# Optimization experiments

Measured on AMD Instinct MI355X. Metric: run time of the kernel, lower is better.

## Reference

```python
import jax, jax.numpy as jnp
import numpy as np

EPS = 1e-5


def _conv1x1_3d(x, w, b):
    # x: [B,C,T,H,W], w: [O,C], b: [O]  (Conv3d with kernel 1)
    return jnp.einsum('bcthw,oc->bothw', x, w) + b[None, :, None, None, None]


def _nonlocal_layer(x, Kw, Kb, Qw, Qb, Vw, Vb, Ow, Ob, gamma, beta, in_dim):
    K = _conv1x1_3d(x, Kw, Kb)
    Q = _conv1x1_3d(x, Qw, Qb)
    V = _conv1x1_3d(x, Vw, Vb)
    B, C, T, H, W = K.shape
    S = T * H * W
    Kf = K.reshape(B, C, S)
    Qf = Q.reshape(B, C, S)
    Vf = V.reshape(B, C, S)
    # KQ[b,s,t] = sum_c K[b,c,s] Q[b,c,t];  attn = softmax over t
    attn = jax.nn.softmax(jnp.einsum('bcs,bct->bst', Kf, Qf) / np.sqrt(in_dim).astype(np.float32), axis=2)
    # original broadcast pattern: (V.view(B,C,S,1) * attn[:,None]).sum(3)
    #   == V[b,c,s] * sum_t attn[b,s,t]  (rows of softmax sum to ~1)
    Vn = Vf * attn.sum(axis=2)[:, None, :]
    Vn = jax.nn.relu(Vn).reshape(B, C, T, H, W)
    O = jax.nn.relu(_conv1x1_3d(Vn, Ow, Ob))
    y = x + O
    # BatchNorm3d in training mode: per-channel batch statistics
    mu = y.mean(axis=(0, 2, 3, 4), keepdims=True)
    var = y.var(axis=(0, 2, 3, 4), keepdims=True)
    return gamma[None, :, None, None, None] * (y - mu) / jnp.sqrt(var + EPS) + beta[None, :, None, None, None]


def _conv_transpose_2x2_s2(x, w, b):
    # torch ConvTranspose2d(k=2, stride=2): weight [Cin, Cout, 2, 2]; output pixels don't overlap
    N, C, H, W = x.shape
    O = w.shape[1]
    y = jnp.einsum('nchw,codk->nohdwk', x, w).reshape(N, O, 2 * H, 2 * W)
    return y + b[None, :, None, None]


def _positional_encoding(S, D):
    position = jnp.arange(S, dtype=jnp.float32)[:, None]
    div_term = jnp.exp(jnp.arange(0, D, 2, dtype=jnp.float32) * (-np.log(10000.0) / D))
    pe = jnp.zeros((S, D), dtype=jnp.float32)
    pe = pe.at[:, 0::2].set(jnp.sin(position * div_term))
    pe = pe.at[:, 1::2].set(jnp.cos(position * div_term))
    return pe  # [S, D]


def setup_inputs() -> dict:
    key = jax.random.key(0)
    ks = jax.random.split(key, 24)
    B, Tc, Hc, Wc = 8, 6, 12, 12
    Tf, Hf, Wf = 4, 12, 12
    Din, Dff, Dout, L = 1024, 512, 128, 2
    s = 0.02
    inp = {
        'context': jax.random.normal(ks[0], (B, Tc, Din, Hc, Wc), jnp.float32),
        'frame': jax.random.normal(ks[1], (B, Tf, Din, Hf, Wf), jnp.float32),
        'nl_Kw': jax.random.normal(ks[2], (L, Dff, Din), jnp.float32) * s,
        'nl_Kb': jnp.zeros((L, Dff), jnp.float32),
        'nl_Qw': jax.random.normal(ks[3], (L, Dff, Din), jnp.float32) * s,
        'nl_Qb': jnp.zeros((L, Dff), jnp.float32),
        'nl_Vw': jax.random.normal(ks[4], (L, Dff, Din), jnp.float32) * s,
        'nl_Vb': jnp.zeros((L, Dff), jnp.float32),
        'nl_Ow': jax.random.normal(ks[5], (L, Din, Dff), jnp.float32) * s,
        'nl_Ob': jnp.zeros((L, Din), jnp.float32),
        'nl_gamma': jnp.ones((L, Din), jnp.float32),
        'nl_beta': jnp.zeros((L, Din), jnp.float32),
        'tp_w': jax.random.normal(ks[6], (Dout, Din, 3, 3, 3), jnp.float32) * s,
        'tp_b': jnp.zeros((Dout,), jnp.float32),
        'up1_w': jax.random.normal(ks[7], (Din, Dff, 2, 2), jnp.float32) * s,
        'up1_b': jnp.zeros((Dff,), jnp.float32),
        'up2_w': jax.random.normal(ks[8], (Dff, Dout, 2, 2), jnp.float32) * s,
        'up2_b': jnp.zeros((Dout,), jnp.float32),
    }
    return inp


def reference(context, frame, nl_Kw, nl_Kb, nl_Qw, nl_Qb, nl_Vw, nl_Vb, nl_Ow, nl_Ob,
              nl_gamma, nl_beta, tp_w, tp_b, up1_w, up1_b, up2_w, up2_b):
    in_dim = context.shape[2]
    out_dim = up2_w.shape[1]
    # ---- non-local layers over context ----
    x = jnp.swapaxes(context, 1, 2)  # [B, C, T, H, W]
    n_layers = nl_Kw.shape[0]
    for l in range(n_layers):
        x = _nonlocal_layer(x, nl_Kw[l], nl_Kb[l], nl_Qw[l], nl_Qb[l], nl_Vw[l], nl_Vb[l],
                            nl_Ow[l], nl_Ob[l], nl_gamma[l], nl_beta[l], in_dim)
    # ---- temporal pool (Conv3d k=3, VALID) + ReLU + global avg pool ----
    g = jax.lax.conv_general_dilated(x, tp_w, (1, 1, 1), 'VALID',
                                     dimension_numbers=('NCDHW', 'OIDHW', 'NCDHW'))
    g = jax.nn.relu(g + tp_b[None, :, None, None, None])
    goal_embed = g.mean(axis=(2, 3, 4))  # [B, out_dim]
    # ---- upsample frame ----
    B, Tf, C, H, W = frame.shape
    fr = frame.reshape(B * Tf, C, H, W)
    h = jax.nn.relu(_conv_transpose_2x2_s2(fr, up1_w, up1_b))
    h = _conv_transpose_2x2_s2(h, up2_w, up2_b)  # [B*Tf, out_dim, 4H, 4W]
    N = B * Tf
    S = H * W * 16
    state_embed = h.reshape(N, out_dim, S)
    # ---- positional encoding on V ----
    pe = _positional_encoding(S, out_dim)  # [S, D]
    V = jnp.transpose(state_embed, (0, 2, 1)) + pe[None, :, :]  # [N, S, D]
    # ---- goal/state attention (note: torch .repeat tiles t-major, kept faithful) ----
    goal_rep = jnp.tile(goal_embed, (Tf, 1))  # [Tf*B, D], index t*B+b
    SG = jnp.einsum('nds,nd->ns', state_embed, goal_rep) / np.sqrt(out_dim).astype(np.float32)
    attn = jax.nn.softmax(SG, axis=1)  # [N, S]
    state_goal_attn = jnp.einsum('ns,nsd->nd', attn, V).reshape(B, Tf, out_dim)
    return (goal_embed, state_goal_attn)
```

## Files before the change

kernel.cpp:

```cpp
#include <hip/hip_runtime.h>
#include <cstddef>
#include <cstdint>


static constexpr int B_ = 8, TC = 6, TF = 4, DIN = 1024, DFF = 512, DOUT = 128;
static constexpr int HWP = 144;
static constexpr int P_CTX = B_ * TC * HWP;
static constexpr int NF = B_ * TF;
static constexpr int P_FRM = NF * HWP;
static constexpr int P_H1 = NF * 24 * 24;
static constexpr int P_H2 = NF * 48 * 48;
static constexpr int S2 = 48 * 48;
static constexpr int NPOS = 3200;

static constexpr size_t OFF_XB   = 0;
static constexpr size_t OFF_YB   = 3538944;
static constexpr size_t OFF_VNB  = 7077888;
static constexpr size_t OFF_WB1  = 8847360;
static constexpr size_t OFF_WB2  = 9371648;
static constexpr size_t OFF_ST   = 9895936;
static constexpr size_t OFF_TWB  = 9900032;
static constexpr size_t OFF_W1B  = 11669504;
static constexpr size_t OFF_W2B  = 12718080;
static constexpr size_t OFF_GP   = 12849152;
static constexpr size_t OFF_R    = 18378752;
static constexpr size_t OFF_HP1B = 18788352;
static constexpr size_t OFF_F0B  = 23506944;
static constexpr size_t OFF_HP2B = 0;
static constexpr size_t OFF_SG   = 12849152;
static constexpr size_t OFF_PE   = 7077888;

typedef __attribute__((ext_vector_type(8))) short bf16x8;
typedef __attribute__((ext_vector_type(4))) float f32x4;
typedef __attribute__((ext_vector_type(4))) unsigned short us4;
typedef __attribute__((ext_vector_type(8))) unsigned short us8;

__device__ __forceinline__ unsigned short f2b(float f) {
    union { float f; uint32_t u; } x{f};
    uint32_t r = x.u + 0x7FFFu + ((x.u >> 16) & 1u);
    return (unsigned short)(r >> 16);
}
__device__ __forceinline__ float b2f(unsigned short u) {
    union { uint32_t u; float f; } x;
    x.u = (uint32_t)u << 16;
    return x.f;
}

#define GL16(g, s)                                                        \
    __builtin_amdgcn_global_load_lds(                                     \
        (const __attribute__((address_space(1))) void*)(g),               \
        (__attribute__((address_space(3))) void*)(s), 16, 0, 0)

static constexpr int PW0 = 4 * 524288;
static constexpr int PW1 = PW0 + 27 * 1024 * 128;
static constexpr int PW2 = PW1 + 4 * 512 * 1024;
static constexpr int PW3 = PW2 + 4 * 128 * 512;
static constexpr int NB_PREP = PW3 / 256;
static constexpr int NB_CTXT = 9 * 16 * (B_ * TC);
static constexpr int NB_FRMT = 9 * 16 * NF;

__device__ __forceinline__ void transpose_body(const float* __restrict__ in,
                                               unsigned short* __restrict__ outB,
                                               int C, int HW, int bx, int by, int bz,
                                               float (*T)[17]) {
    int tid = threadIdx.x;
    int tx = tid & 15, ty = tid >> 4;
    int f = bz, hw0 = bx * 16, c0 = by * 64;
#pragma unroll
    for (int i = 0; i < 4; ++i)
        T[ty + 16 * i][tx] = in[((size_t)f * C + c0 + ty + 16 * i) * HW + hw0 + tx];
    __syncthreads();
#pragma unroll
    for (int i = 0; i < 4; ++i)
        outB[((size_t)f * HW + hw0 + ty) * C + c0 + tx + 16 * i] = f2b(T[tx + 16 * i][ty]);
}

__global__ __launch_bounds__(256) void prep_all(
    const float* __restrict__ Vw, const float* __restrict__ Ow,
    const float* __restrict__ tp, const float* __restrict__ u1w,
    const float* __restrict__ u2w,
    const float* __restrict__ context, const float* __restrict__ frame,
    unsigned short* __restrict__ WB1, unsigned short* __restrict__ WB2,
    unsigned short* __restrict__ TWB, unsigned short* __restrict__ W1B,
    unsigned short* __restrict__ W2B,
    unsigned short* __restrict__ XB, unsigned short* __restrict__ F0B) {
    __shared__ float T[64][17];
    int b = blockIdx.x;
    if (b < NB_PREP) {
        int t = b * 256 + threadIdx.x;
        if (t < PW0) {
            int which = t >> 19;
            int r = t & 524287;
            int kr = r & 7;
            int layer = which >> 1;
            if ((which & 1) == 0) {
                int o = (r >> 3) & 511, kg = (r >> 3) >> 9;
                WB1[(size_t)layer * 524288 + r] =
                    f2b(Vw[(size_t)layer * 524288 + (size_t)o * 1024 + kg * 8 + kr]);
            } else {
                int o = (r >> 3) & 1023, kg = (r >> 3) >> 10;
                WB2[(size_t)layer * 524288 + r] =
                    f2b(Ow[(size_t)layer * 524288 + (size_t)o * 512 + kg * 8 + kr]);
            }
        } else if (t < PW1) {
            int r = t - PW0;
            int kr = r & 7, o = (r >> 3) & 127, kg = (r >> 10) & 127, tap = r >> 17;
            int c = kg * 8 + kr;
            TWB[r] = f2b(tp[((size_t)o * 1024 + c) * 27 + tap]);
        } else if (t < PW2) {
            int r = t - PW1;
            int kr = r & 7, o = (r >> 3) % 512;
            int rest = (r >> 3) / 512;
            int kg = rest & 127, d = rest >> 7;
            W1B[r] = f2b(u1w[((size_t)(kg * 8 + kr) * 512 + o) * 4 + d]);
        } else if (t < PW3) {
            int r = t - PW2;
            int kr = r & 7, o = (r >> 3) & 127;
            int rest = (r >> 3) >> 7;
            int kg = rest & 63, d = rest >> 6;
            W2B[r] = f2b(u2w[((size_t)(kg * 8 + kr) * 128 + o) * 4 + d]);
        }
    } else if (b < NB_PREP + NB_CTXT) {
        int bb = b - NB_PREP;
        transpose_body(context, XB, DIN, HWP, bb % 9, (bb / 9) % 16, bb / 144, T);
    } else {
        int bb = b - NB_PREP - NB_CTXT;
        transpose_body(frame, F0B, DIN, HWP, bb % 9, (bb / 9) % 16, bb / 144, T);
    }
}

template <int EPI, int REMAP, int GATHER, int MT>
__device__ __forceinline__ void gemm_body(
    const unsigned short* __restrict__ A, const unsigned short* __restrict__ Bp,
    const float* __restrict__ bias, const unsigned short* __restrict__ resid,
    void* __restrict__ Cv, int M, int N, int K,
    size_t bStrideZ, size_t cStrideZ,
    int inW, int inHW, int outW, int outSPP,
    int bx, int by, int bz,
    unsigned short* AlP, unsigned short* BlP, int* sPix) {
    constexpr int MI = MT / 32;
    constexpr int AL = MT / 64;
    constexpr int ASZ = MT * 32;
    int tid = threadIdx.x;
    int w = tid >> 6, l = tid & 63;
    int m0 = by * MT, n0 = bx * 128;
    int z = bz;
    const unsigned short* Bpz = Bp + (size_t)z * bStrideZ;

    if (GATHER) {
        if (tid < MT) {
            int pos = m0 + tid;
            int ww = pos % 10;
            int r = pos / 10;
            int h = r % 10;
            r /= 10;
            int t = r & 3, b = r >> 2;
            int dt = z / 9, rr = z - dt * 9;
            int doff = dt * 144 + (rr / 3) * 12 + (rr % 3);
            sPix[tid] = ((b * 6 + t) * 12 + h) * 12 + ww + doff;
        }
        __syncthreads();
    }

    int wr = w >> 1, wc = w & 1;
    int l15 = l & 15, lg = l >> 4;

    float bv[4];
#pragma unroll
    for (int ni = 0; ni < 4; ++ni)
        bv[ni] = (EPI & 1) ? bias[n0 + wc * 64 + ni * 16 + l15] : 0.f;
    asm volatile("s_waitcnt vmcnt(0)" ::: "memory");

    const unsigned short* ag[AL];
    int aoff[AL];
#pragma unroll
    for (int a = 0; a < AL; ++a) {
        int row = l + a * 64;
        int grow = GATHER ? sPix[row] : (m0 + row);
        ag[a] = A + (size_t)grow * K + w * 8;
        aoff[a] = (w * MT + row) * 8;
    }
    int bkg = tid >> 7, bn = tid & 127;
    const unsigned short* bg0 = Bpz + ((size_t)bkg * N + n0 + bn) * 8;
    const unsigned short* bg1 = Bpz + ((size_t)(bkg + 2) * N + n0 + bn) * 8;
    const int boff0 = tid * 8, boff1 = (tid + 256) * 8;
    size_t bstep = (size_t)32 * N;

    f32x4 acc[MI][4];
#pragma unroll
    for (int mi = 0; mi < MI; ++mi)
#pragma unroll
        for (int ni = 0; ni < 4; ++ni) acc[mi][ni] = (f32x4){0.f, 0.f, 0.f, 0.f};

    int nt = K >> 5;
#pragma unroll
    for (int a = 0; a < AL; ++a) { GL16(ag[a], &AlP[aoff[a]]); ag[a] += 32; }
    GL16(bg0, &BlP[boff0]);
    GL16(bg1, &BlP[boff1]);
    bg0 += bstep; bg1 += bstep;
#pragma unroll
    for (int a = 0; a < AL; ++a) { GL16(ag[a], &AlP[ASZ + aoff[a]]); ag[a] += 32; }
    GL16(bg0, &BlP[4096 + boff0]);
    GL16(bg1, &BlP[4096 + boff1]);
    bg0 += bstep; bg1 += bstep;

    int bc = 0, sb = 2;
    for (int t = 0; t < nt; ++t) {
        __builtin_amdgcn_s_barrier();
        if (t + 2 < nt) {
#pragma unroll
            for (int a = 0; a < AL; ++a) { GL16(ag[a], &AlP[sb * ASZ + aoff[a]]); ag[a] += 32; }
            GL16(bg0, &BlP[sb * 4096 + boff0]);
            GL16(bg1, &BlP[sb * 4096 + boff1]);
            bg0 += bstep; bg1 += bstep;
            if (MT == 128)
                asm volatile("s_waitcnt vmcnt(8)" ::: "memory");
            else
                asm volatile("s_waitcnt vmcnt(6)" ::: "memory");
        } else if (t + 2 == nt) {
            if (MT == 128)
                asm volatile("s_waitcnt vmcnt(4)" ::: "memory");
            else
                asm volatile("s_waitcnt vmcnt(3)" ::: "memory");
        } else {
            asm volatile("s_waitcnt vmcnt(0)" ::: "memory");
        }
        __builtin_amdgcn_sched_barrier(0);
        bf16x8 af[MI], bf[4];
#pragma unroll
        for (int mi = 0; mi < MI; ++mi)
            af[mi] = *(const bf16x8*)&AlP[bc * ASZ + (lg * MT + wr * (MT / 2) + mi * 16 + l15) * 8];
#pragma unroll
        for (int ni = 0; ni < 4; ++ni)
            bf[ni] = *(const bf16x8*)&BlP[bc * 4096 + (lg * 128 + wc * 64 + ni * 16 + l15) * 8];
        __builtin_amdgcn_s_setprio(1);
#pragma unroll
        for (int mi = 0; mi < MI; ++mi)
#pragma unroll
            for (int ni = 0; ni < 4; ++ni)
                acc[mi][ni] = __builtin_amdgcn_mfma_f32_16x16x32_bf16(
                    af[mi], bf[ni], acc[mi][ni], 0, 0, 0);
        __builtin_amdgcn_s_setprio(0);
        __builtin_amdgcn_sched_barrier(0);
        bc = (bc == 2) ? 0 : bc + 1;
        sb = (sb == 2) ? 0 : sb + 1;
    }

    float* Cf = (float*)Cv + (size_t)z * cStrideZ;
    unsigned short* Cb = (unsigned short*)Cv + (size_t)z * cStrideZ;
#pragma unroll
    for (int mi = 0; mi < MI; ++mi) {
#pragma unroll
        for (int r = 0; r < 4; ++r) {
            int m = m0 + wr * (MT / 2) + mi * 16 + lg * 4 + r;
            int orow = m;
            if (REMAP) {
                int ni_ = m / inHW;
                int rem = m - ni_ * inHW;
                int h = rem / inW, ww = rem - h * inW;
                orow = ni_ * outSPP + (2 * h + (z >> 1)) * outW + (2 * ww + (z & 1));
            }
#pragma unroll
            for (int ni = 0; ni < 4; ++ni) {
                int n = n0 + wc * 64 + ni * 16 + l15;
                float v = acc[mi][ni][r] + bv[ni];
                if (EPI & 2) v = fmaxf(v, 0.f);
                if (EPI & 4) v += b2f(resid[(size_t)m * N + n]);
                if (EPI & 8)
                    Cb[(size_t)orow * N + n] = f2b(v);
                else
                    Cf[(size_t)orow * N + n] = v;
            }
        }
    }
}

template <int EPI, int REMAP, int GATHER, int MT>
__global__ __launch_bounds__(256) void gemm_mfma(
    const unsigned short* __restrict__ A, const unsigned short* __restrict__ Bp,
    const float* __restrict__ bias, const unsigned short* __restrict__ resid,
    void* __restrict__ Cv, int M, int N, int K,
    size_t bStrideZ, size_t cStrideZ,
    int inW, int inHW, int outW, int outSPP) {
    __shared__ unsigned short Al[3 * MT * 32];
    __shared__ unsigned short Bl[3 * 128 * 32];
    __shared__ int sPix[MT];
    gemm_body<EPI, REMAP, GATHER, MT>(A, Bp, bias, resid, Cv, M, N, K,
                                      bStrideZ, cStrideZ, inW, inHW, outW, outSPP,
                                      blockIdx.x, blockIdx.y, blockIdx.z,
                                      Al, Bl, sPix);
}

__global__ __launch_bounds__(256) void conv3_up1(
    const unsigned short* __restrict__ XB, const unsigned short* __restrict__ TWB,
    unsigned short* __restrict__ GP,
    const unsigned short* __restrict__ F0B, const unsigned short* __restrict__ W1B,
    const float* __restrict__ u1b, unsigned short* __restrict__ HP1B) {
    __shared__ unsigned short Al[3 * 128 * 32];
    __shared__ unsigned short Bl[3 * 128 * 32];
    __shared__ int sPix[128];
    if (blockIdx.x < 680) {
        int xcd = blockIdx.x & 7, k = blockIdx.x >> 3;
        int wcnt = (xcd < 3) ? 85 : 84;
        if (k >= wcnt) return;
        int wk = (xcd < 3) ? xcd * 85 + k : 255 + (xcd - 3) * 84 + k;
        gemm_body<8, 0, 1, 128>(XB, TWB, nullptr, nullptr, GP, NPOS, DOUT, DIN,
                                (size_t)DIN / 8 * DOUT * 8, (size_t)NPOS * DOUT,
                                0, 0, 0, 0, 0, wk / 27, wk % 27, Al, Bl, sPix);
    } else {
        int b = blockIdx.x - 680;
        gemm_body<11, 1, 0, 128>(F0B, W1B, u1b, nullptr, HP1B, P_FRM, DFF, DIN,
                                 (size_t)DIN / 8 * DFF * 8, 0, 12, 144, 24, 576,
                                 b & 3, (b >> 2) % 36, b / 144, Al, Bl, sPix);
    }
}

__global__ __launch_bounds__(256) void up2_tail(
    const unsigned short* __restrict__ HP1B, const unsigned short* __restrict__ W2B,
    const float* __restrict__ u2b, unsigned short* __restrict__ HP2B,
    const unsigned short* __restrict__ Gp, const float* __restrict__ tpb,
    float* __restrict__ R, float* __restrict__ PE) {
    __shared__ unsigned short Al[3 * 128 * 32];
    __shared__ unsigned short Bl[3 * 128 * 32];
    __shared__ int sPix[128];
    int b = blockIdx.x;
    if (b < 576) {
        gemm_body<9, 1, 0, 128>(HP1B, W2B, u2b, nullptr, HP2B, P_H1, DOUT, DFF,
                                (size_t)DFF / 8 * DOUT * 8, 0, 24, 576, 48, 2304,
                                0, b % 144, b / 144, Al, Bl, sPix);
    } else if (b < 2176) {
        int idx = (b - 576) * 256 + threadIdx.x;
        float s = 0.f;
        for (int tap = 0; tap < 27; ++tap) s += b2f(Gp[(size_t)tap * (NPOS * 128) + idx]);
        R[idx] = fmaxf(s + tpb[idx & 127], 0.f);
    } else {
        int idx = (b - 2176) * 256 + threadIdx.x;
        int s = idx >> 7, d = idx & 127;
        float freq = expf(-(float)(d & ~1) * (9.210340371976184f / 128.f));
        float ang = (float)s * freq;
        PE[idx] = (d & 1) ? cosf(ang) : sinf(ang);
    }
}

__global__ __launch_bounds__(128) void goal_reduce(const float* __restrict__ R,
                                                   float* __restrict__ out) {
    int b = blockIdx.x, o = threadIdx.x;
    float s = 0.f;
    for (int i = 0; i < 400; ++i) s += R[(size_t)(b * 400 + i) * 128 + o];
    out[b * 128 + o] = s * (1.f / 400.f);
}


__global__ __launch_bounds__(256) void bn_stats_b(const unsigned short* __restrict__ YB,
                                                  float* __restrict__ st) {
    int tid = threadIdx.x;
    int p0 = blockIdx.x * 64;
    int c0 = tid * 4;
    float s[4] = {0, 0, 0, 0}, q[4] = {0, 0, 0, 0};
    for (int pp = 0; pp < 64; ++pp) {
        us4 y = *(const us4*)(YB + (size_t)(p0 + pp) * 1024 + c0);
#pragma unroll
        for (int j = 0; j < 4; ++j) {
            float v = b2f(y[j]);
            s[j] += v;
            q[j] += v * v;
        }
    }
#pragma unroll
    for (int j = 0; j < 4; ++j) {
        atomicAdd(&st[c0 + j], s[j]);
        atomicAdd(&st[1024 + c0 + j], q[j]);
    }
}

__global__ __launch_bounds__(256) void bn_final(float* __restrict__ st,
                                                const float* __restrict__ gamma,
                                                const float* __restrict__ beta) {
    int c = blockIdx.x * 256 + threadIdx.x;
    if (c >= 1024) return;
    const float invn = 1.f / 6912.f;
    float mean = st[c] * invn;
    float var = st[1024 + c] * invn - mean * mean;
    float sc = gamma[c] * rsqrtf(var + 1e-5f);
    st[2048 + c] = sc;
    st[3072 + c] = beta[c] - mean * sc;
}

__global__ __launch_bounds__(256) void bn_apply_b(const unsigned short* __restrict__ YB,
                                                  unsigned short* __restrict__ XB,
                                                  const float* __restrict__ st) {
    const float* scale = st + 2048;
    const float* shift = st + 3072;
    int idx = blockIdx.x * 256 + threadIdx.x;
    int c0 = (idx & 255) << 2;
    us4 y = ((const us4*)YB)[idx];
    us4 o;
#pragma unroll
    for (int j = 0; j < 4; ++j) o[j] = f2b(b2f(y[j]) * scale[c0 + j] + shift[c0 + j]);
    ((us4*)XB)[idx] = o;
}


__global__ __launch_bounds__(256) void attn_logits(const unsigned short* __restrict__ Hp2,
                                                   const float* __restrict__ out,
                                                   float* __restrict__ SG) {
    int n = blockIdx.y;
    int tid = threadIdx.x;
    int s = blockIdx.x * 16 + (tid >> 4);
    int l16 = tid & 15;
    us8 row = *((const us8*)(Hp2 + ((size_t)n * S2 + s) * 128) + l16);
    const float* g = out + (n & 7) * 128 + l16 * 8;
    float dot = 0.f;
#pragma unroll
    for (int i = 0; i < 8; ++i) dot += b2f(row[i]) * g[i];
    dot += __shfl_xor(dot, 1);
    dot += __shfl_xor(dot, 2);
    dot += __shfl_xor(dot, 4);
    dot += __shfl_xor(dot, 8);
    if (l16 == 0) SG[(size_t)n * S2 + s] = dot * 0.0883883476483184f;
}

__global__ __launch_bounds__(256) void attn_softmax(float* __restrict__ SG) {
    __shared__ float red[256];
    int n = blockIdx.x, tid = threadIdx.x;
    float* row = SG + (size_t)n * S2;
    float v[9];
    float lmax = -3.4e38f;
#pragma unroll
    for (int i = 0; i < 9; ++i) {
        v[i] = row[tid + 256 * i];
        lmax = fmaxf(lmax, v[i]);
    }
    red[tid] = lmax;
    __syncthreads();
    for (int off = 128; off > 0; off >>= 1) {
        if (tid < off) red[tid] = fmaxf(red[tid], red[tid + off]);
        __syncthreads();
    }
    float m = red[0];
    __syncthreads();
    float ls = 0.f;
#pragma unroll
    for (int i = 0; i < 9; ++i) {
        v[i] = expf(v[i] - m);
        ls += v[i];
    }
    red[tid] = ls;
    __syncthreads();
    for (int off = 128; off > 0; off >>= 1) {
        if (tid < off) red[tid] += red[tid + off];
        __syncthreads();
    }
    float inv = 1.f / red[0];
#pragma unroll
    for (int i = 0; i < 9; ++i) row[tid + 256 * i] = v[i] * inv;
}

__global__ __launch_bounds__(256) void attn_pv(const unsigned short* __restrict__ Hp2,
                                               const float* __restrict__ SG,
                                               const float* __restrict__ PE,
                                               float* __restrict__ out) {
    int n = blockIdx.y;
    int sb = blockIdx.x;
    int tid = threadIdx.x;
    int d = tid & 127, half = tid >> 7;
    int s0 = sb * 128 + half * 64;
    const float* att = SG + (size_t)n * S2;
    float acc = 0.f;
    for (int i = 0; i < 64; ++i) {
        int s = s0 + i;
        acc += att[s] * (b2f(Hp2[((size_t)n * S2 + s) * 128 + d]) + PE[(size_t)s * 128 + d]);
    }
    atomicAdd(&out[1024 + n * 128 + d], acc);
}


extern "C" void kernel_launch(void* const* d_in, const int* in_sizes, int n_in,
                              void* d_out, int out_size, void* d_ws, size_t ws_size,
                              hipStream_t stream) {
    const float* context = (const float*)d_in[0];
    const float* frame = (const float*)d_in[1];
    const float* Vw = (const float*)d_in[6];
    const float* Vb = (const float*)d_in[7];
    const float* Ow = (const float*)d_in[8];
    const float* Ob = (const float*)d_in[9];
    const float* gamma = (const float*)d_in[10];
    const float* beta = (const float*)d_in[11];
    const float* tpw = (const float*)d_in[12];
    const float* tpb = (const float*)d_in[13];
    const float* u1w = (const float*)d_in[14];
    const float* u1b = (const float*)d_in[15];
    const float* u2w = (const float*)d_in[16];
    const float* u2b = (const float*)d_in[17];
    float* ws = (float*)d_ws;
    float* out = (float*)d_out;

    unsigned short* XB = (unsigned short*)(ws + OFF_XB);
    unsigned short* YB = (unsigned short*)(ws + OFF_YB);
    unsigned short* VNB = (unsigned short*)(ws + OFF_VNB);
    unsigned short* WB1 = (unsigned short*)(ws + OFF_WB1);
    unsigned short* WB2 = (unsigned short*)(ws + OFF_WB2);
    float* ST = ws + OFF_ST;
    unsigned short* TWB = (unsigned short*)(ws + OFF_TWB);
    unsigned short* W1B = (unsigned short*)(ws + OFF_W1B);
    unsigned short* W2B = (unsigned short*)(ws + OFF_W2B);
    unsigned short* GP = (unsigned short*)(ws + OFF_GP);
    float* R = ws + OFF_R;
    unsigned short* F0B = (unsigned short*)(ws + OFF_F0B);
    unsigned short* HP1B = (unsigned short*)(ws + OFF_HP1B);
    unsigned short* HP2B = (unsigned short*)(ws + OFF_HP2B);
    float* SG = ws + OFF_SG;
    float* PE = ws + OFF_PE;

    prep_all<<<NB_PREP + NB_CTXT + NB_FRMT, 256, 0, stream>>>(
        Vw, Ow, tpw, u1w, u2w, context, frame, WB1, WB2, TWB, W1B, W2B, XB, F0B);

    for (int l = 0; l < 2; ++l) {
        gemm_mfma<11, 0, 0, 64><<<dim3(DFF / 128, P_CTX / 64, 1), 256, 0, stream>>>(
            XB, WB1 + (size_t)l * 524288, Vb + l * DFF, nullptr, VNB,
            P_CTX, DFF, DIN, 0, 0, 0, 0, 0, 0);
        gemm_mfma<15, 0, 0, 128><<<dim3(DIN / 128, P_CTX / 128, 1), 256, 0, stream>>>(
            VNB, WB2 + (size_t)l * 524288, Ob + l * DIN, XB, YB,
            P_CTX, DIN, DFF, 0, 0, 0, 0, 0, 0);
        hipMemsetAsync(ST, 0, 2048 * sizeof(float), stream);
        bn_stats_b<<<P_CTX / 64, 256, 0, stream>>>(YB, ST);
        bn_final<<<4, 256, 0, stream>>>(ST, gamma + l * DIN, beta + l * DIN);
        bn_apply_b<<<(P_CTX * DIN / 4) / 256, 256, 0, stream>>>(YB, XB, ST);
    }

    conv3_up1<<<680 + 576, 256, 0, stream>>>(XB, TWB, GP, F0B, W1B, u1b, HP1B);

    up2_tail<<<576 + 1600 + 1152, 256, 0, stream>>>(HP1B, W2B, u2b, HP2B,
                                                    GP, tpb, R, PE);
    goal_reduce<<<8, 128, 0, stream>>>(R, out);
    hipMemsetAsync(out + 1024, 0, (size_t)NF * 128 * sizeof(float), stream);

    attn_logits<<<dim3(S2 / 16, NF), 256, 0, stream>>>(HP2B, out, SG);
    attn_softmax<<<NF, 256, 0, stream>>>(SG);
    attn_pv<<<dim3(18, NF), 256, 0, stream>>>(HP2B, SG, PE, out);
}
```

Baseline: 286.4 us.

## Fuse BN stats into GEMM epilogue, group conv taps, fold memsets into kernels

Batch-norm sum and sum-of-squares are now accumulated in the second GEMM's epilogue through shared-memory and global atomics, which removes the separate stats pass over YB. The stats memsets move into the prep kernel and the output memset moves into up2_tail, removing two memset launches. The 3D conv now gives each block three taps and accumulates them in registers, writing 9 partials instead of 27. This cuts partial-sum traffic and the reduction loop, at the cost of fewer, longer blocks (232 vs 680) and extra atomics in the epilogue.

Measured after the change: 279.7 us. 2.3% less time.

```diff
diff --git a/kernel.cpp b/kernel.cpp
--- a/kernel.cpp
+++ b/kernel.cpp
@@ -18,16 +18,16 @@
 static constexpr size_t OFF_VNB  = 7077888;
 static constexpr size_t OFF_WB1  = 8847360;
 static constexpr size_t OFF_WB2  = 9371648;
-static constexpr size_t OFF_ST   = 9895936;
 static constexpr size_t OFF_TWB  = 9900032;
 static constexpr size_t OFF_W1B  = 11669504;
 static constexpr size_t OFF_W2B  = 12718080;
+static constexpr size_t OFF_ST   = 12849152;
 static constexpr size_t OFF_GP   = 12849152;
 static constexpr size_t OFF_R    = 18378752;
 static constexpr size_t OFF_HP1B = 18788352;
 static constexpr size_t OFF_F0B  = 23506944;
 static constexpr size_t OFF_HP2B = 0;
-static constexpr size_t OFF_SG   = 12849152;
+static constexpr size_t OFF_SG   = 14692352;
 static constexpr size_t OFF_PE   = 7077888;
 
 typedef __attribute__((ext_vector_type(8))) short bf16x8;
@@ -58,6 +58,7 @@
 static constexpr int NB_PREP = PW3 / 256;
 static constexpr int NB_CTXT = 9 * 16 * (B_ * TC);
 static constexpr int NB_FRMT = 9 * 16 * NF;
+static constexpr int NB_STZ  = 32;
 
 __device__ __forceinline__ void transpose_body(const float* __restrict__ in,
                                                unsigned short* __restrict__ outB,
@@ -83,7 +84,8 @@
     unsigned short* __restrict__ WB1, unsigned short* __restrict__ WB2,
     unsigned short* __restrict__ TWB, unsigned short* __restrict__ W1B,
     unsigned short* __restrict__ W2B,
-    unsigned short* __restrict__ XB, unsigned short* __restrict__ F0B) {
+    unsigned short* __restrict__ XB, unsigned short* __restrict__ F0B,
+    float* __restrict__ ST) {
     __shared__ float T[64][17];
     int b = blockIdx.x;
     if (b < NB_PREP) {
@@ -123,9 +125,12 @@
     } else if (b < NB_PREP + NB_CTXT) {
         int bb = b - NB_PREP;
         transpose_body(context, XB, DIN, HWP, bb % 9, (bb / 9) % 16, bb / 144, T);
-    } else {
+    } else if (b < NB_PREP + NB_CTXT + NB_FRMT) {
         int bb = b - NB_PREP - NB_CTXT;
         transpose_body(frame, F0B, DIN, HWP, bb % 9, (bb / 9) % 16, bb / 144, T);
+    } else {
+        int idx = (b - NB_PREP - NB_CTXT - NB_FRMT) * 256 + threadIdx.x;
+        ST[idx] = 0.f;
     }
 }
 
@@ -133,7 +138,7 @@
 __device__ __forceinline__ void gemm_body(
     const unsigned short* __restrict__ A, const unsigned short* __restrict__ Bp,
     const float* __restrict__ bias, const unsigned short* __restrict__ resid,
-    void* __restrict__ Cv, int M, int N, int K,
+    void* __restrict__ Cv, float* __restrict__ stats, int M, int N, int K,
     size_t bStrideZ, size_t cStrideZ,
     int inW, int inHW, int outW, int outSPP,
     int bx, int by, int bz,
@@ -248,6 +253,7 @@
 
     float* Cf = (float*)Cv + (size_t)z * cStrideZ;
     unsigned short* Cb = (unsigned short*)Cv + (size_t)z * cStrideZ;
+    float sacc[4] = {0, 0, 0, 0}, qacc[4] = {0, 0, 0, 0};
 #pragma unroll
     for (int mi = 0; mi < MI; ++mi) {
 #pragma unroll
@@ -266,6 +272,7 @@
                 float v = acc[mi][ni][r] + bv[ni];
                 if (EPI & 2) v = fmaxf(v, 0.f);
                 if (EPI & 4) v += b2f(resid[(size_t)m * N + n]);
+                if (EPI & 16) { sacc[ni] += v; qacc[ni] += v * v; }
                 if (EPI & 8)
                     Cb[(size_t)orow * N + n] = f2b(v);
                 else
@@ -273,19 +280,36 @@
             }
         }
     }
+    if (EPI & 16) {
+        __syncthreads();
+        float* sred = (float*)AlP;
+        sred[tid] = 0.f;
+        __syncthreads();
+#pragma unroll
+        for (int ni = 0; ni < 4; ++ni) {
+            int c = wc * 64 + ni * 16 + l15;
+            atomicAdd(&sred[c], sacc[ni]);
+            atomicAdd(&sred[128 + c], qacc[ni]);
+        }
+        __syncthreads();
+        if (tid < 128)
+            atomicAdd(&stats[n0 + tid], sred[tid]);
+        else
+            atomicAdd(&stats[1024 + n0 + (tid & 127)], sred[tid]);
+    }
 }
 
 template <int EPI, int REMAP, int GATHER, int MT>
 __global__ __launch_bounds__(256) void gemm_mfma(
     const unsigned short* __restrict__ A, const unsigned short* __restrict__ Bp,
     const float* __restrict__ bias, const unsigned short* __restrict__ resid,
-    void* __restrict__ Cv, int M, int N, int K,
+    void* __restrict__ Cv, float* __restrict__ stats, int M, int N, int K,
     size_t bStrideZ, size_t cStrideZ,
     int inW, int inHW, int outW, int outSPP) {
     __shared__ unsigned short Al[3 * MT * 32];
     __shared__ unsigned short Bl[3 * 128 * 32];
     __shared__ int sPix[MT];
-    gemm_body<EPI, REMAP, GATHER, MT>(A, Bp, bias, resid, Cv, M, N, K,
+    gemm_body<EPI, REMAP, GATHER, MT>(A, Bp, bias, resid, Cv, stats, M, N, K,
                                       bStrideZ, cStrideZ, inW, inHW, outW, outSPP,
                                       blockIdx.x, blockIdx.y, blockIdx.z,
                                       Al, Bl, sPix);
@@ -299,46 +323,150 @@
     __shared__ unsigned short Al[3 * 128 * 32];
     __shared__ unsigned short Bl[3 * 128 * 32];
     __shared__ int sPix[128];
-    if (blockIdx.x < 680) {
-        int xcd = blockIdx.x & 7, k = blockIdx.x >> 3;
-        int wcnt = (xcd < 3) ? 85 : 84;
-        if (k >= wcnt) return;
-        int wk = (xcd < 3) ? xcd * 85 + k : 255 + (xcd - 3) * 84 + k;
-        gemm_body<8, 0, 1, 128>(XB, TWB, nullptr, nullptr, GP, NPOS, DOUT, DIN,
-                                (size_t)DIN / 8 * DOUT * 8, (size_t)NPOS * DOUT,
-                                0, 0, 0, 0, 0, wk / 27, wk % 27, Al, Bl, sPix);
-    } else {
-        int b = blockIdx.x - 680;
-        gemm_body<11, 1, 0, 128>(F0B, W1B, u1b, nullptr, HP1B, P_FRM, DFF, DIN,
+    if (blockIdx.x >= 232) {
+        int b = blockIdx.x - 232;
+        gemm_body<11, 1, 0, 128>(F0B, W1B, u1b, nullptr, HP1B, nullptr,
+                                 P_FRM, DFF, DIN,
                                  (size_t)DIN / 8 * DFF * 8, 0, 12, 144, 24, 576,
                                  b & 3, (b >> 2) % 36, b / 144, Al, Bl, sPix);
-    }
+        return;
+    }
+    int xcd = blockIdx.x & 7, k = blockIdx.x >> 3;
+    int wcnt = (xcd == 0) ? 29 : 28;
+    if (k >= wcnt) return;
+    int wk = (xcd == 0) ? k : 29 + (xcd - 1) * 28 + k;
+    int tg = wk / 25, mt = wk % 25;
+    int m0 = mt * 128;
+    int tid = threadIdx.x;
+    int w = tid >> 6, l = tid & 63;
+    int wr = w >> 1, wc = w & 1;
+    int l15 = l & 15, lg = l >> 4;
+
+    f32x4 acc[4][4];
+#pragma unroll
+    for (int mi = 0; mi < 4; ++mi)
+#pragma unroll
+        for (int ni = 0; ni < 4; ++ni) acc[mi][ni] = (f32x4){0.f, 0.f, 0.f, 0.f};
+
+    asm volatile("s_waitcnt vmcnt(0)" ::: "memory");
+
+    for (int t3 = 0; t3 < 3; ++t3) {
+        int tap = tg * 3 + t3;
+        __syncthreads();
+        if (tid < 128) {
+            int pos = m0 + tid;
+            int ww = pos % 10;
+            int r = pos / 10;
+            int h = r % 10;
+            r /= 10;
+            int t = r & 3, b = r >> 2;
+            int dt = tap / 9, rr = tap - dt * 9;
+            int doff = dt * 144 + (rr / 3) * 12 + (rr % 3);
+            sPix[tid] = ((b * 6 + t) * 12 + h) * 12 + ww + doff;
+        }
+        __syncthreads();
+        const unsigned short* Bpz = TWB + (size_t)tap * (DIN / 8 * DOUT * 8);
+        const unsigned short* ag0 = XB + (size_t)sPix[l] * DIN + w * 8;
+        const unsigned short* ag1 = XB + (size_t)sPix[l + 64] * DIN + w * 8;
+        const int a0off = (w * 128 + l) * 8;
+        const int a1off = (w * 128 + l + 64) * 8;
+        int bkg = tid >> 7, bn = tid & 127;
+        const unsigned short* bg0 = Bpz + ((size_t)bkg * DOUT + bn) * 8;
+        const unsigned short* bg1 = Bpz + ((size_t)(bkg + 2) * DOUT + bn) * 8;
+        const int boff0 = tid * 8, boff1 = (tid + 256) * 8;
+        size_t bstep = (size_t)32 * DOUT;
+
+        GL16(ag0, &Al[a0off]); ag0 += 32;
+        GL16(ag1, &Al[a1off]); ag1 += 32;
+        GL16(bg0, &Bl[boff0]);
+        GL16(bg1, &Bl[boff1]);
+        bg0 += bstep; bg1 += bstep;
+        GL16(ag0, &Al[4096 + a0off]); ag0 += 32;
+        GL16(ag1, &Al[4096 + a1off]); ag1 += 32;
+        GL16(bg0, &Bl[4096 + boff0]);
+        GL16(bg1, &Bl[4096 + boff1]);
+        bg0 += bstep; bg1 += bstep;
+
+        int bc = 0, sb = 2;
+        int nt = DIN >> 5;
+        for (int t = 0; t < nt; ++t) {
+            __builtin_amdgcn_s_barrier();
+            if (t + 2 < nt) {
+                GL16(ag0, &Al[sb * 4096 + a0off]); ag0 += 32;
+                GL16(ag1, &Al[sb * 4096 + a1off]); ag1 += 32;
+                GL16(bg0, &Bl[sb * 4096 + boff0]);
+                GL16(bg1, &Bl[sb * 4096 + boff1]);
+                bg0 += bstep; bg1 += bstep;
+                asm volatile("s_waitcnt vmcnt(8)" ::: "memory");
+            } else if (t + 2 == nt) {
+                asm volatile("s_waitcnt vmcnt(4)" ::: "memory");
+            } else {
+                asm volatile("s_waitcnt vmcnt(0)" ::: "memory");
+            }
+            __builtin_amdgcn_sched_barrier(0);
+            bf16x8 af[4], bf[4];
+#pragma unroll
+            for (int mi = 0; mi < 4; ++mi)
+                af[mi] = *(const bf16x8*)&Al[bc * 4096 + (lg * 128 + wr * 64 + mi * 16 + l15) * 8];
+#pragma unroll
+            for (int ni = 0; ni < 4; ++ni)
+                bf[ni] = *(const bf16x8*)&Bl[bc * 4096 + (lg * 128 + wc * 64 + ni * 16 + l15) * 8];
+            __builtin_amdgcn_s_setprio(1);
+#pragma unroll
+            for (int mi = 0; mi < 4; ++mi)
+#pragma unroll
+                for (int ni = 0; ni < 4; ++ni)
+                    acc[mi][ni] = __builtin_amdgcn_mfma_f32_16x16x32_bf16(
+                        af[mi], bf[ni], acc[mi][ni], 0, 0, 0);
+            __builtin_amdgcn_s_setprio(0);
+            __builtin_amdgcn_sched_barrier(0);
+            bc = (bc == 2) ? 0 : bc + 1;
+            sb = (sb == 2) ? 0 : sb + 1;
+        }
+    }
+
+    unsigned short* Cb = GP + (size_t)tg * (NPOS * DOUT);
+#pragma unroll
+    for (int mi = 0; mi < 4; ++mi)
+#pragma unroll
+        for (int r = 0; r < 4; ++r) {
+            int m = m0 + wr * 64 + mi * 16 + lg * 4 + r;
+#pragma unroll
+            for (int ni = 0; ni < 4; ++ni) {
+                int n = wc * 64 + ni * 16 + l15;
+                Cb[(size_t)m * DOUT + n] = f2b(acc[mi][ni][r]);
+            }
+        }
 }
 
 __global__ __launch_bounds__(256) void up2_tail(
     const unsigned short* __restrict__ HP1B, const unsigned short* __restrict__ W2B,
     const float* __restrict__ u2b, unsigned short* __restrict__ HP2B,
     const unsigned short* __restrict__ Gp, const float* __restrict__ tpb,
-    float* __restrict__ R, float* __restrict__ PE) {
+    float* __restrict__ R, float* __restrict__ PE, float* __restrict__ out) {
     __shared__ unsigned short Al[3 * 128 * 32];
     __shared__ unsigned short Bl[3 * 128 * 32];
     __shared__ int sPix[128];
     int b = blockIdx.x;
     if (b < 576) {
-        gemm_body<9, 1, 0, 128>(HP1B, W2B, u2b, nullptr, HP2B, P_H1, DOUT, DFF,
+        gemm_body<9, 1, 0, 128>(HP1B, W2B, u2b, nullptr, HP2B, nullptr,
+                                P_H1, DOUT, DFF,
                                 (size_t)DFF / 8 * DOUT * 8, 0, 24, 576, 48, 2304,
                                 0, b % 144, b / 144, Al, Bl, sPix);
     } else if (b < 2176) {
         int idx = (b - 576) * 256 + threadIdx.x;
         float s = 0.f;
-        for (int tap = 0; tap < 27; ++tap) s += b2f(Gp[(size_t)tap * (NPOS * 128) + idx]);
+        for (int tgi = 0; tgi < 9; ++tgi) s += b2f(Gp[(size_t)tgi * (NPOS * 128) + idx]);
         R[idx] = fmaxf(s + tpb[idx & 127], 0.f);
-    } else {
+    } else if (b < 3328) {
         int idx = (b - 2176) * 256 + threadIdx.x;
         int s = idx >> 7, d = idx & 127;
         float freq = expf(-(float)(d & ~1) * (9.210340371976184f / 128.f));
         float ang = (float)s * freq;
         PE[idx] = (d & 1) ? cosf(ang) : sinf(ang);
+    } else {
+        int idx = (b - 3328) * 256 + threadIdx.x;
+        out[1024 + idx] = 0.f;
     }
 }
 
@@ -350,28 +478,6 @@
     out[b * 128 + o] = s * (1.f / 400.f);
 }
 
-
-__global__ __launch_bounds__(256) void bn_stats_b(const unsigned short* __restrict__ YB,
-                                                  float* __restrict__ st) {
-    int tid = threadIdx.x;
-    int p0 = blockIdx.x * 64;
-    int c0 = tid * 4;
-    float s[4] = {0, 0, 0, 0}, q[4] = {0, 0, 0, 0};
-    for (int pp = 0; pp < 64; ++pp) {
-        us4 y = *(const us4*)(YB + (size_t)(p0 + pp) * 1024 + c0);
-#pragma unroll
-        for (int j = 0; j < 4; ++j) {
-            float v = b2f(y[j]);
-            s[j] += v;
-            q[j] += v * v;
-        }
-    }
-#pragma unroll
-    for (int j = 0; j < 4; ++j) {
-        atomicAdd(&st[c0 + j], s[j]);
-        atomicAdd(&st[1024 + c0 + j], q[j]);
-    }
-}
 
 __global__ __launch_bounds__(256) void bn_final(float* __restrict__ st,
                                                 const float* __restrict__ gamma,
@@ -512,28 +618,27 @@
     float* SG = ws + OFF_SG;
     float* PE = ws + OFF_PE;
 
-    prep_all<<<NB_PREP + NB_CTXT + NB_FRMT, 256, 0, stream>>>(
-        Vw, Ow, tpw, u1w, u2w, context, frame, WB1, WB2, TWB, W1B, W2B, XB, F0B);
+    prep_all<<<NB_PREP + NB_CTXT + NB_FRMT + NB_STZ, 256, 0, stream>>>(
+        Vw, Ow, tpw, u1w, u2w, context, frame, WB1, WB2, TWB, W1B, W2B,
+        XB, F0B, ST);
 
     for (int l = 0; l < 2; ++l) {
+        float* STl = ST + (size_t)l * 4096;
         gemm_mfma<11, 0, 0, 64><<<dim3(DFF / 128, P_CTX / 64, 1), 256, 0, stream>>>(
-            XB, WB1 + (size_t)l * 524288, Vb + l * DFF, nullptr, VNB,
+            XB, WB1 + (size_t)l * 524288, Vb + l * DFF, nullptr, VNB, nullptr,
             P_CTX, DFF, DIN, 0, 0, 0, 0, 0, 0);
-        gemm_mfma<15, 0, 0, 128><<<dim3(DIN / 128, P_CTX / 128, 1), 256, 0, stream>>>(
-            VNB, WB2 + (size_t)l * 524288, Ob + l * DIN, XB, YB,
+        gemm_mfma<31, 0, 0, 128><<<dim3(DIN / 128, P_CTX / 128, 1), 256, 0, stream>>>(
+            VNB, WB2 + (size_t)l * 524288, Ob + l * DIN, XB, YB, STl,
             P_CTX, DIN, DFF, 0, 0, 0, 0, 0, 0);
-        hipMemsetAsync(ST, 0, 2048 * sizeof(float), stream);
-        bn_stats_b<<<P_CTX / 64, 256, 0, stream>>>(YB, ST);
-        bn_final<<<4, 256, 0, stream>>>(ST, gamma + l * DIN, beta + l * DIN);
-        bn_apply_b<<<(P_CTX * DIN / 4) / 256, 256, 0, stream>>>(YB, XB, ST);
-    }
-
-    conv3_up1<<<680 + 576, 256, 0, stream>>>(XB, TWB, GP, F0B, W1B, u1b, HP1B);
-
-    up2_tail<<<576 + 1600 + 1152, 256, 0, stream>>>(HP1B, W2B, u2b, HP2B,
-                                                    GP, tpb, R, PE);
+        bn_final<<<4, 256, 0, stream>>>(STl, gamma + l * DIN, beta + l * DIN);
+        bn_apply_b<<<(P_CTX * DIN / 4) / 256, 256, 0, stream>>>(YB, XB, STl);
+    }
+
+    conv3_up1<<<232 + 576, 256, 0, stream>>>(XB, TWB, GP, F0B, W1B, u1b, HP1B);
+
+    up2_tail<<<576 + 1600 + 1152 + 16, 256, 0, stream>>>(HP1B, W2B, u2b, HP2B,
+                                                         GP, tpb, R, PE, out);
     goal_reduce<<<8, 128, 0, stream>>>(R, out);
-    hipMemsetAsync(out + 1024, 0, (size_t)NF * 128 * sizeof(float), stream);
 
     attn_logits<<<dim3(S2 / 16, NF), 256, 0, stream>>>(HP2B, out, SG);
     attn_softmax<<<NF, 256, 0, stream>>>(SG);
```
